# Kernel optimization log

Hardware: AMD Instinct MI355X
Metric: run time of the kernel (lower is better)

## Reference

```python
import jax, jax.numpy as jnp
import numpy as np

DIM = 4096
N_ITERS = 20
TEMP = 1.0
NOISE_FACTOR = 1.0
EPS = 1e-10


def setup_inputs() -> dict:
    key = jax.random.key(0)
    k1, k2 = jax.random.split(key)
    # logits initialized as log(I + 1e-5) + 0.01*randn, per reset_parameters
    identity = jnp.eye(DIM, dtype=jnp.float32)
    logits = jnp.log(identity + 1e-05) + 0.01 * jax.random.normal(k1, (DIM, DIM), dtype=jnp.float32)
    # uniform noise; Gumbel transform applied inside reference (matches gumbel_noise)
    noise = jax.random.uniform(k2, (DIM, DIM), dtype=jnp.float32)
    return {"logits": logits, "noise": noise}


def reference(logits, noise):
    # Gumbel noise from uniform samples
    g = -jnp.log(-jnp.log(noise + EPS) + EPS) * NOISE_FACTOR
    log_alpha = (logits + g) / TEMP

    def body(la, _):
        la = la - jax.scipy.special.logsumexp(la, axis=1, keepdims=True)  # row normalize
        la = la - jax.scipy.special.logsumexp(la, axis=0, keepdims=True)  # col normalize
        return la, None

    log_alpha, _ = jax.lax.scan(body, log_alpha, None, length=N_ITERS)
    return jnp.exp(log_alpha)
```

## Files before the change

kernel.cpp:

```cpp
#include <hip/hip_runtime.h>
#include <math.h>

#define DIM   4096
#define NITER 20
#define EPSF  1e-10f
#define NB    256
#define NT    1024
#define RPB   16
#define NRG   16

typedef __attribute__((ext_vector_type(4))) _Float16 half4;

__device__ __forceinline__ void st_co(float* p, float v) {
    __hip_atomic_store(p, v, __ATOMIC_RELAXED, __HIP_MEMORY_SCOPE_AGENT);
}
__device__ __forceinline__ float ld_co(const float* p) {
    return __hip_atomic_load(p, __ATOMIC_RELAXED, __HIP_MEMORY_SCOPE_AGENT);
}

__device__ __forceinline__ void gridbarrier(unsigned* bar, int b, unsigned idx) {
    __syncthreads();
    if (threadIdx.x == 0) {
        unsigned* gen  = bar;
        unsigned* root = bar + 16;
        unsigned* cnt  = bar + 32 + 16 * (b & 7);
        unsigned a = __hip_atomic_fetch_add(cnt, 1u, __ATOMIC_RELAXED, __HIP_MEMORY_SCOPE_AGENT);
        if (a == 32u * (idx + 1u) - 1u) {
            unsigned a2 = __hip_atomic_fetch_add(root, 1u, __ATOMIC_RELAXED, __HIP_MEMORY_SCOPE_AGENT);
            if (a2 == 8u * (idx + 1u) - 1u) {
                __hip_atomic_fetch_add(gen, 1u, __ATOMIC_RELAXED, __HIP_MEMORY_SCOPE_AGENT);
            }
        }
        while (__hip_atomic_load(gen, __ATOMIC_RELAXED, __HIP_MEMORY_SCOPE_AGENT) < idx + 1u)
            __builtin_amdgcn_s_sleep(1);
    }
    __syncthreads();
}

__global__ void zero_bar(unsigned* bar) {
    if (threadIdx.x < 256) bar[threadIdx.x] = 0u;
}

__global__ __launch_bounds__(NT, 4) void sinkhorn_lds(
        const float* __restrict__ logits, const float* __restrict__ noise,
        float* __restrict__ out, float* __restrict__ cg, unsigned* __restrict__ bar) {
    __shared__ _Float16 lm[RPB][DIM];
    __shared__ float    lc[DIM];
    __shared__ float    rbc[RPB];

    const int t = threadIdx.x;
    const int b = blockIdx.x;
    const int wave = t >> 6, lane = t & 63;
    const int g0 = b * RPB;
    float* part = out;

#pragma unroll
    for (int r = 0; r < RPB; ++r) {
        const float4 l = *(const float4*)(logits + (size_t)(g0 + r) * DIM + 4 * t);
        const float4 u = *(const float4*)(noise  + (size_t)(g0 + r) * DIM + 4 * t);
        half4 h;
        h.x = (_Float16)(l.x - __logf(-__logf(u.x + EPSF) + EPSF));
        h.y = (_Float16)(l.y - __logf(-__logf(u.y + EPSF) + EPSF));
        h.z = (_Float16)(l.z - __logf(-__logf(u.z + EPSF) + EPSF));
        h.w = (_Float16)(l.w - __logf(-__logf(u.w + EPSF) + EPSF));
        *(half4*)&lm[r][4 * t] = h;
    }
    *(float4*)&lc[4 * t] = make_float4(0.f, 0.f, 0.f, 0.f);
    __syncthreads();

    for (int it = 0; it < NITER; ++it) {
        {
            float m = -1e30f;
#pragma unroll
            for (int k = 0; k < 16; ++k) {
                const int col = (k * 64 + lane) * 4;
                const half4  h  = *(const half4*)&lm[wave][col];
                const float4 c4 = *(const float4*)&lc[col];
                m = fmaxf(m, fmaxf(fmaxf((float)h.x - c4.x, (float)h.y - c4.y),
                                   fmaxf((float)h.z - c4.z, (float)h.w - c4.w)));
            }
#pragma unroll
            for (int o = 1; o < 64; o <<= 1) m = fmaxf(m, __shfl_xor(m, o, 64));
            float s = 0.f;
#pragma unroll
            for (int k = 0; k < 16; ++k) {
                const int col = (k * 64 + lane) * 4;
                const half4  h  = *(const half4*)&lm[wave][col];
                const float4 c4 = *(const float4*)&lc[col];
                s += __expf((float)h.x - c4.x - m) + __expf((float)h.y - c4.y - m)
                   + __expf((float)h.z - c4.z - m) + __expf((float)h.w - c4.w - m);
            }
#pragma unroll
            for (int o = 1; o < 64; o <<= 1) s += __shfl_xor(s, o, 64);
            if (lane == 0) rbc[wave] = m + __logf(s);
        }
        __syncthreads();

        {
            float4 mx = make_float4(-1e30f, -1e30f, -1e30f, -1e30f);
#pragma unroll
            for (int r2 = 0; r2 < RPB; ++r2) {
                const half4 h = *(const half4*)&lm[r2][4 * t];
                const float rr = rbc[r2];
                mx.x = fmaxf(mx.x, (float)h.x - rr);
                mx.y = fmaxf(mx.y, (float)h.y - rr);
                mx.z = fmaxf(mx.z, (float)h.z - rr);
                mx.w = fmaxf(mx.w, (float)h.w - rr);
            }
            float4 sm = make_float4(0.f, 0.f, 0.f, 0.f);
#pragma unroll
            for (int r2 = 0; r2 < RPB; ++r2) {
                const half4 h = *(const half4*)&lm[r2][4 * t];
                const float rr = rbc[r2];
                sm.x += __expf((float)h.x - rr - mx.x);
                sm.y += __expf((float)h.y - rr - mx.y);
                sm.z += __expf((float)h.z - rr - mx.z);
                sm.w += __expf((float)h.w - rr - mx.w);
            }
            float* pp = part + (size_t)b * DIM + 4 * t;
            st_co(pp + 0, mx.x + __logf(sm.x));
            st_co(pp + 1, mx.y + __logf(sm.y));
            st_co(pp + 2, mx.z + __logf(sm.z));
            st_co(pp + 3, mx.w + __logf(sm.w));
        }

        gridbarrier(bar, b, 2u * it);

        {
            const int jj = g0 + wave;
            const float p0 = ld_co(part + (size_t)(lane      ) * DIM + jj);
            const float p1 = ld_co(part + (size_t)(lane +  64) * DIM + jj);
            const float p2 = ld_co(part + (size_t)(lane + 128) * DIM + jj);
            const float p3 = ld_co(part + (size_t)(lane + 192) * DIM + jj);
            float m = fmaxf(fmaxf(p0, p1), fmaxf(p2, p3));
#pragma unroll
            for (int o = 1; o < 64; o <<= 1) m = fmaxf(m, __shfl_xor(m, o, 64));
            float s = __expf(p0 - m) + __expf(p1 - m) + __expf(p2 - m) + __expf(p3 - m);
#pragma unroll
            for (int o = 1; o < 64; o <<= 1) s += __shfl_xor(s, o, 64);
            if (lane == 0) st_co(cg + jj, m + __logf(s));
        }

        gridbarrier(bar, b, 2u * it + 1u);

        lc[4 * t + 0] = ld_co(cg + 4 * t + 0);
        lc[4 * t + 1] = ld_co(cg + 4 * t + 1);
        lc[4 * t + 2] = ld_co(cg + 4 * t + 2);
        lc[4 * t + 3] = ld_co(cg + 4 * t + 3);
        __syncthreads();
    }

    const float4 c4f = *(const float4*)&lc[4 * t];
#pragma unroll
    for (int r = 0; r < RPB; ++r) {
        const half4 h = *(const half4*)&lm[r][4 * t];
        const float rr = rbc[r];
        float4 o;
        o.x = __expf((float)h.x - rr - c4f.x);
        o.y = __expf((float)h.y - rr - c4f.y);
        o.z = __expf((float)h.z - rr - c4f.z);
        o.w = __expf((float)h.w - rr - c4f.w);
        *(float4*)(out + (size_t)(g0 + r) * DIM + 4 * t) = o;
    }
}

__device__ __forceinline__ float waveMaxF(float v) {
#pragma unroll
    for (int o = 32; o > 0; o >>= 1) v = fmaxf(v, __shfl_down(v, o, 64));
    return v;
}
__device__ __forceinline__ float waveSumF(float v) {
#pragma unroll
    for (int o = 32; o > 0; o >>= 1) v += __shfl_down(v, o, 64);
    return v;
}

__global__ __launch_bounds__(256) void init_k(const float* __restrict__ logits,
                                              const float* __restrict__ noise,
                                              float* __restrict__ L0,
                                              float* __restrict__ c) {
    int idx = blockIdx.x * blockDim.x + threadIdx.x;
    int stride = gridDim.x * blockDim.x;
    const float4* l4 = (const float4*)logits;
    const float4* n4 = (const float4*)noise;
    float4* o4 = (float4*)L0;
    for (int p = idx; p < DIM * DIM / 4; p += stride) {
        float4 l = l4[p];
        float4 u = n4[p];
        float4 o;
        o.x = l.x - __logf(-__logf(u.x + EPSF) + EPSF);
        o.y = l.y - __logf(-__logf(u.y + EPSF) + EPSF);
        o.z = l.z - __logf(-__logf(u.z + EPSF) + EPSF);
        o.w = l.w - __logf(-__logf(u.w + EPSF) + EPSF);
        o4[p] = o;
    }
    if (idx < DIM) c[idx] = 0.0f;
}

__global__ __launch_bounds__(256) void row_lse(const float* __restrict__ L0,
                                               const float* __restrict__ c,
                                               float* __restrict__ r) {
    __shared__ float red[8];
    const int row = blockIdx.x;
    const int t = threadIdx.x;
    const float4* a4 = (const float4*)(L0 + (size_t)row * DIM);
    const float4* c4 = (const float4*)c;
    float v[16];
    float m = -INFINITY;
#pragma unroll
    for (int k = 0; k < 4; ++k) {
        float4 a  = a4[t + k * 256];
        float4 cc = c4[t + k * 256];
        v[4 * k + 0] = a.x - cc.x;
        v[4 * k + 1] = a.y - cc.y;
        v[4 * k + 2] = a.z - cc.z;
        v[4 * k + 3] = a.w - cc.w;
        m = fmaxf(m, fmaxf(fmaxf(v[4 * k], v[4 * k + 1]), fmaxf(v[4 * k + 2], v[4 * k + 3])));
    }
    m = waveMaxF(m);
    const int lane = t & 63, wid = t >> 6;
    if (lane == 0) red[wid] = m;
    __syncthreads();
    const float bm = fmaxf(fmaxf(red[0], red[1]), fmaxf(red[2], red[3]));
    float s = 0.0f;
#pragma unroll
    for (int q = 0; q < 16; ++q) s += __expf(v[q] - bm);
    s = waveSumF(s);
    if (lane == 0) red[4 + wid] = s;
    __syncthreads();
    if (t == 0) r[row] = bm + __logf(red[4] + red[5] + red[6] + red[7]);
}

__global__ __launch_bounds__(1024) void col_partial(const float* __restrict__ L0,
                                                    const float* __restrict__ r,
                                                    float2* __restrict__ part) {
    __shared__ float sr[256];
    __shared__ float smm[1024];
    __shared__ float sms[1024];
    const int g = blockIdx.x, h = blockIdx.y;
    const int tc = threadIdx.x & 255;
    const int ln = threadIdx.x >> 8;
    if (threadIdx.x < 256) sr[threadIdx.x] = r[h * 256 + threadIdx.x];
    __syncthreads();
    const int j = g * 256 + tc;
    float m = -INFINITY, s = 0.0f;
#pragma unroll 4
    for (int k = 0; k < 64; ++k) {
        int ii = k * 4 + ln;
        float v = L0[(size_t)(h * 256 + ii) * DIM + j] - sr[ii];
        float nm = fmaxf(m, v);
        s = s * __expf(m - nm) + __expf(v - nm);
        m = nm;
    }
    smm[threadIdx.x] = m;
    sms[threadIdx.x] = s;
    __syncthreads();
    if (threadIdx.x < 256) {
        float m0 = smm[tc], m1 = smm[tc + 256], m2 = smm[tc + 512], m3 = smm[tc + 768];
        float M = fmaxf(fmaxf(m0, m1), fmaxf(m2, m3));
        float S = sms[tc] * __expf(m0 - M) + sms[tc + 256] * __expf(m1 - M) +
                  sms[tc + 512] * __expf(m2 - M) + sms[tc + 768] * __expf(m3 - M);
        part[h * DIM + j] = make_float2(M, S);
    }
}

__global__ __launch_bounds__(256) void col_combine(const float2* __restrict__ part,
                                                   float* __restrict__ c) {
    int j = blockIdx.x * 256 + threadIdx.x;
    float pm[NRG], ps[NRG];
    float M = -INFINITY;
#pragma unroll
    for (int h = 0; h < NRG; ++h) {
        float2 p = part[h * DIM + j];
        pm[h] = p.x; ps[h] = p.y;
        M = fmaxf(M, p.x);
    }
    float S = 0.0f;
#pragma unroll
    for (int h = 0; h < NRG; ++h) S += ps[h] * __expf(pm[h] - M);
    c[j] = M + __logf(S);
}

__global__ __launch_bounds__(256) void final_exp(float* __restrict__ L0,
                                                 const float* __restrict__ r,
                                                 const float* __restrict__ c) {
    const float4* c4 = (const float4*)c;
    float4* a4 = (float4*)L0;
    int idx = blockIdx.x * blockDim.x + threadIdx.x;
    int stride = gridDim.x * blockDim.x;
    for (int p = idx; p < DIM * DIM / 4; p += stride) {
        int i  = p >> 10;
        int j4 = p & 1023;
        float4 a = a4[p];
        float rrv = r[i];
        float4 ccv = c4[j4];
        a.x = __expf(a.x - rrv - ccv.x);
        a.y = __expf(a.y - rrv - ccv.y);
        a.z = __expf(a.z - rrv - ccv.z);
        a.w = __expf(a.w - rrv - ccv.w);
        a4[p] = a;
    }
}

extern "C" void kernel_launch(void* const* d_in, const int* in_sizes, int n_in,
                              void* d_out, int out_size, void* d_ws, size_t ws_size,
                              hipStream_t stream) {
    const float* logits = (const float*)d_in[0];
    const float* noise  = (const float*)d_in[1];
    float* out = (float*)d_out;
    float* cg  = (float*)d_ws;
    unsigned* bar = (unsigned*)((char*)d_ws + 16384);

    zero_bar<<<1, 256, 0, stream>>>(bar);
    void* args[] = { (void*)&logits, (void*)&noise, (void*)&out, (void*)&cg, (void*)&bar };
    hipError_t err = hipLaunchCooperativeKernel((const void*)sinkhorn_lds,
                                                dim3(NB), dim3(NT), args, 0, stream);
    if (err != hipSuccess) {
        float* ws = (float*)d_ws;
        float*  r    = ws;
        float*  cf   = ws + DIM;
        float2* part = (float2*)(ws + 2 * DIM);
        init_k<<<4096, 256, 0, stream>>>(logits, noise, out, cf);
        for (int t = 0; t < NITER; ++t) {
            row_lse<<<DIM, 256, 0, stream>>>(out, cf, r);
            col_partial<<<dim3(16, 16), 1024, 0, stream>>>(out, r, part);
            col_combine<<<16, 256, 0, stream>>>(part, cf);
        }
        final_exp<<<4096, 256, 0, stream>>>(out, r, cf);
    }
}
```

Before: 596.8 us.

## Switch Sinkhorn to multiplicative scaling form with bf16 kernel matrix

Replaces the log-domain Sinkhorn iterations with the equivalent multiplicative form. The matrix exp(log_alpha) is stored once in LDS as bf16, and the row and column scaling vectors are updated with reciprocals of plain sums, which removes the per-element exp, log and max passes from every iteration. The grid barrier is also flattened: each block bumps one of 8 counters and spins on all 8 counters instead of going through a two-level root/generation counter. Cross-block stores and loads are widened to 64-bit. The cost is numerical: bf16 storage and no max-subtraction can lose precision or overflow or underflow for extreme logits, with identity-like logits spanning roughly e^-11.5 up to 1 times Gumbel factors.

```diff
diff --git a/kernel.cpp b/kernel.cpp
--- a/kernel.cpp
+++ b/kernel.cpp
@@ -9,7 +9,17 @@
 #define RPB   16
 #define NRG   16
 
-typedef __attribute__((ext_vector_type(4))) _Float16 half4;
+typedef __attribute__((ext_vector_type(4))) unsigned short ushort4_t;
+
+__device__ __forceinline__ float bf2f(unsigned short b) {
+    unsigned int x = ((unsigned int)b) << 16;
+    return __builtin_bit_cast(float, x);
+}
+__device__ __forceinline__ unsigned short f2bf(float f) {
+    unsigned int x = __builtin_bit_cast(unsigned int, f);
+    x += 0x7fffu + ((x >> 16) & 1u);
+    return (unsigned short)(x >> 16);
+}
 
 __device__ __forceinline__ void st_co(float* p, float v) {
     __hip_atomic_store(p, v, __ATOMIC_RELAXED, __HIP_MEMORY_SCOPE_AGENT);
@@ -17,21 +27,31 @@
 __device__ __forceinline__ float ld_co(const float* p) {
     return __hip_atomic_load(p, __ATOMIC_RELAXED, __HIP_MEMORY_SCOPE_AGENT);
 }
+__device__ __forceinline__ void st_co2(float* p, float a, float b) {
+    unsigned long long v =
+        ((unsigned long long)__builtin_bit_cast(unsigned int, b) << 32) |
+        (unsigned long long)__builtin_bit_cast(unsigned int, a);
+    __hip_atomic_store((unsigned long long*)p, v, __ATOMIC_RELAXED, __HIP_MEMORY_SCOPE_AGENT);
+}
+__device__ __forceinline__ float2 ld_co2(const float* p) {
+    unsigned long long v =
+        __hip_atomic_load((const unsigned long long*)p, __ATOMIC_RELAXED, __HIP_MEMORY_SCOPE_AGENT);
+    float2 r;
+    r.x = __builtin_bit_cast(float, (unsigned int)(v & 0xffffffffull));
+    r.y = __builtin_bit_cast(float, (unsigned int)(v >> 32));
+    return r;
+}
 
 __device__ __forceinline__ void gridbarrier(unsigned* bar, int b, unsigned idx) {
     __syncthreads();
-    if (threadIdx.x == 0) {
-        unsigned* gen  = bar;
-        unsigned* root = bar + 16;
-        unsigned* cnt  = bar + 32 + 16 * (b & 7);
-        unsigned a = __hip_atomic_fetch_add(cnt, 1u, __ATOMIC_RELAXED, __HIP_MEMORY_SCOPE_AGENT);
-        if (a == 32u * (idx + 1u) - 1u) {
-            unsigned a2 = __hip_atomic_fetch_add(root, 1u, __ATOMIC_RELAXED, __HIP_MEMORY_SCOPE_AGENT);
-            if (a2 == 8u * (idx + 1u) - 1u) {
-                __hip_atomic_fetch_add(gen, 1u, __ATOMIC_RELAXED, __HIP_MEMORY_SCOPE_AGENT);
-            }
-        }
-        while (__hip_atomic_load(gen, __ATOMIC_RELAXED, __HIP_MEMORY_SCOPE_AGENT) < idx + 1u)
+    if (threadIdx.x < 8) {
+        const unsigned tgt = 32u * (idx + 1u);
+        if (threadIdx.x == 0) {
+            __hip_atomic_fetch_add(bar + 32 + 16 * (b & 7), 1u,
+                                   __ATOMIC_RELAXED, __HIP_MEMORY_SCOPE_AGENT);
+        }
+        unsigned* c = bar + 32 + 16 * threadIdx.x;
+        while (__hip_atomic_load(c, __ATOMIC_RELAXED, __HIP_MEMORY_SCOPE_AGENT) < tgt)
             __builtin_amdgcn_s_sleep(1);
     }
     __syncthreads();
@@ -41,12 +61,12 @@
     if (threadIdx.x < 256) bar[threadIdx.x] = 0u;
 }
 
-__global__ __launch_bounds__(NT, 4) void sinkhorn_lds(
+__global__ __launch_bounds__(NT, 4) void sinkhorn_mult(
         const float* __restrict__ logits, const float* __restrict__ noise,
         float* __restrict__ out, float* __restrict__ cg, unsigned* __restrict__ bar) {
-    __shared__ _Float16 lm[RPB][DIM];
-    __shared__ float    lc[DIM];
-    __shared__ float    rbc[RPB];
+    __shared__ unsigned short lm[RPB][DIM];
+    __shared__ float          lw[DIM];
+    __shared__ float          ru[RPB];
 
     const int t = threadIdx.x;
     const int b = blockIdx.x;
@@ -58,108 +78,88 @@
     for (int r = 0; r < RPB; ++r) {
         const float4 l = *(const float4*)(logits + (size_t)(g0 + r) * DIM + 4 * t);
         const float4 u = *(const float4*)(noise  + (size_t)(g0 + r) * DIM + 4 * t);
-        half4 h;
-        h.x = (_Float16)(l.x - __logf(-__logf(u.x + EPSF) + EPSF));
-        h.y = (_Float16)(l.y - __logf(-__logf(u.y + EPSF) + EPSF));
-        h.z = (_Float16)(l.z - __logf(-__logf(u.z + EPSF) + EPSF));
-        h.w = (_Float16)(l.w - __logf(-__logf(u.w + EPSF) + EPSF));
-        *(half4*)&lm[r][4 * t] = h;
-    }
-    *(float4*)&lc[4 * t] = make_float4(0.f, 0.f, 0.f, 0.f);
+        ushort4_t e;
+        e.x = f2bf(__expf(l.x) * __builtin_amdgcn_rcpf(EPSF - __logf(u.x + EPSF)));
+        e.y = f2bf(__expf(l.y) * __builtin_amdgcn_rcpf(EPSF - __logf(u.y + EPSF)));
+        e.z = f2bf(__expf(l.z) * __builtin_amdgcn_rcpf(EPSF - __logf(u.z + EPSF)));
+        e.w = f2bf(__expf(l.w) * __builtin_amdgcn_rcpf(EPSF - __logf(u.w + EPSF)));
+        *(ushort4_t*)&lm[r][4 * t] = e;
+    }
+    *(float4*)&lw[4 * t] = make_float4(1.f, 1.f, 1.f, 1.f);
     __syncthreads();
 
     for (int it = 0; it < NITER; ++it) {
         {
-            float m = -1e30f;
+            float4 s4 = make_float4(0.f, 0.f, 0.f, 0.f);
 #pragma unroll
             for (int k = 0; k < 16; ++k) {
                 const int col = (k * 64 + lane) * 4;
-                const half4  h  = *(const half4*)&lm[wave][col];
-                const float4 c4 = *(const float4*)&lc[col];
-                m = fmaxf(m, fmaxf(fmaxf((float)h.x - c4.x, (float)h.y - c4.y),
-                                   fmaxf((float)h.z - c4.z, (float)h.w - c4.w)));
+                const ushort4_t e  = *(const ushort4_t*)&lm[wave][col];
+                const float4    w4 = *(const float4*)&lw[col];
+                s4.x += bf2f(e.x) * w4.x;
+                s4.y += bf2f(e.y) * w4.y;
+                s4.z += bf2f(e.z) * w4.z;
+                s4.w += bf2f(e.w) * w4.w;
             }
-#pragma unroll
-            for (int o = 1; o < 64; o <<= 1) m = fmaxf(m, __shfl_xor(m, o, 64));
-            float s = 0.f;
-#pragma unroll
-            for (int k = 0; k < 16; ++k) {
-                const int col = (k * 64 + lane) * 4;
-                const half4  h  = *(const half4*)&lm[wave][col];
-                const float4 c4 = *(const float4*)&lc[col];
-                s += __expf((float)h.x - c4.x - m) + __expf((float)h.y - c4.y - m)
-                   + __expf((float)h.z - c4.z - m) + __expf((float)h.w - c4.w - m);
-            }
+            float s = (s4.x + s4.y) + (s4.z + s4.w);
 #pragma unroll
             for (int o = 1; o < 64; o <<= 1) s += __shfl_xor(s, o, 64);
-            if (lane == 0) rbc[wave] = m + __logf(s);
+            if (lane == 0) ru[wave] = __builtin_amdgcn_rcpf(s);
         }
         __syncthreads();
 
         {
-            float4 mx = make_float4(-1e30f, -1e30f, -1e30f, -1e30f);
+            float4 p = make_float4(0.f, 0.f, 0.f, 0.f);
 #pragma unroll
             for (int r2 = 0; r2 < RPB; ++r2) {
-                const half4 h = *(const half4*)&lm[r2][4 * t];
-                const float rr = rbc[r2];
-                mx.x = fmaxf(mx.x, (float)h.x - rr);
-                mx.y = fmaxf(mx.y, (float)h.y - rr);
-                mx.z = fmaxf(mx.z, (float)h.z - rr);
-                mx.w = fmaxf(mx.w, (float)h.w - rr);
-            }
-            float4 sm = make_float4(0.f, 0.f, 0.f, 0.f);
-#pragma unroll
-            for (int r2 = 0; r2 < RPB; ++r2) {
-                const half4 h = *(const half4*)&lm[r2][4 * t];
-                const float rr = rbc[r2];
-                sm.x += __expf((float)h.x - rr - mx.x);
-                sm.y += __expf((float)h.y - rr - mx.y);
-                sm.z += __expf((float)h.z - rr - mx.z);
-                sm.w += __expf((float)h.w - rr - mx.w);
+                const ushort4_t e = *(const ushort4_t*)&lm[r2][4 * t];
+                const float uu = ru[r2];
+                p.x += bf2f(e.x) * uu;
+                p.y += bf2f(e.y) * uu;
+                p.z += bf2f(e.z) * uu;
+                p.w += bf2f(e.w) * uu;
             }
             float* pp = part + (size_t)b * DIM + 4 * t;
-            st_co(pp + 0, mx.x + __logf(sm.x));
-            st_co(pp + 1, mx.y + __logf(sm.y));
-            st_co(pp + 2, mx.z + __logf(sm.z));
-            st_co(pp + 3, mx.w + __logf(sm.w));
+            st_co2(pp + 0, p.x, p.y);
+            st_co2(pp + 2, p.z, p.w);
         }
 
         gridbarrier(bar, b, 2u * it);
 
         {
             const int jj = g0 + wave;
-            const float p0 = ld_co(part + (size_t)(lane      ) * DIM + jj);
-            const float p1 = ld_co(part + (size_t)(lane +  64) * DIM + jj);
-            const float p2 = ld_co(part + (size_t)(lane + 128) * DIM + jj);
-            const float p3 = ld_co(part + (size_t)(lane + 192) * DIM + jj);
-            float m = fmaxf(fmaxf(p0, p1), fmaxf(p2, p3));
-#pragma unroll
-            for (int o = 1; o < 64; o <<= 1) m = fmaxf(m, __shfl_xor(m, o, 64));
-            float s = __expf(p0 - m) + __expf(p1 - m) + __expf(p2 - m) + __expf(p3 - m);
+            float s = ld_co(part + (size_t)(lane      ) * DIM + jj)
+                    + ld_co(part + (size_t)(lane +  64) * DIM + jj)
+                    + ld_co(part + (size_t)(lane + 128) * DIM + jj)
+                    + ld_co(part + (size_t)(lane + 192) * DIM + jj);
 #pragma unroll
             for (int o = 1; o < 64; o <<= 1) s += __shfl_xor(s, o, 64);
-            if (lane == 0) st_co(cg + jj, m + __logf(s));
+            if (lane == 0) st_co(cg + jj, s);
         }
 
         gridbarrier(bar, b, 2u * it + 1u);
 
-        lc[4 * t + 0] = ld_co(cg + 4 * t + 0);
-        lc[4 * t + 1] = ld_co(cg + 4 * t + 1);
-        lc[4 * t + 2] = ld_co(cg + 4 * t + 2);
-        lc[4 * t + 3] = ld_co(cg + 4 * t + 3);
+        {
+            const float2 a = ld_co2(cg + 4 * t + 0);
+            const float2 c2 = ld_co2(cg + 4 * t + 2);
+            lw[4 * t + 0] = __builtin_amdgcn_rcpf(a.x);
+            lw[4 * t + 1] = __builtin_amdgcn_rcpf(a.y);
+            lw[4 * t + 2] = __builtin_amdgcn_rcpf(c2.x);
+            lw[4 * t + 3] = __builtin_amdgcn_rcpf(c2.y);
+        }
         __syncthreads();
     }
 
-    const float4 c4f = *(const float4*)&lc[4 * t];
+    const float4 w4 = *(const float4*)&lw[4 * t];
 #pragma unroll
     for (int r = 0; r < RPB; ++r) {
-        const half4 h = *(const half4*)&lm[r][4 * t];
-        const float rr = rbc[r];
+        const ushort4_t e = *(const ushort4_t*)&lm[r][4 * t];
+        const float uu = ru[r];
         float4 o;
-        o.x = __expf((float)h.x - rr - c4f.x);
-        o.y = __expf((float)h.y - rr - c4f.y);
-        o.z = __expf((float)h.z - rr - c4f.z);
-        o.w = __expf((float)h.w - rr - c4f.w);
+        o.x = bf2f(e.x) * (uu * w4.x);
+        o.y = bf2f(e.y) * (uu * w4.y);
+        o.z = bf2f(e.z) * (uu * w4.z);
+        o.w = bf2f(e.w) * (uu * w4.w);
         *(float4*)(out + (size_t)(g0 + r) * DIM + 4 * t) = o;
     }
 }
@@ -313,7 +313,7 @@
 
     zero_bar<<<1, 256, 0, stream>>>(bar);
     void* args[] = { (void*)&logits, (void*)&noise, (void*)&out, (void*)&cg, (void*)&bar };
-    hipError_t err = hipLaunchCooperativeKernel((const void*)sinkhorn_lds,
+    hipError_t err = hipLaunchCooperativeKernel((const void*)sinkhorn_mult,
                                                 dim3(NB), dim3(NT), args, 0, stream);
     if (err != hipSuccess) {
         float* ws = (float*)d_ws;
```

Result: faster. 552.1 us (-7.5%).
